# Kernel optimization log

Measured on AMD Instinct MI355X. Metric: run time of the kernel, lower is better.

## Reference

```python
import jax, jax.numpy as jnp
import numpy as np

EMB, HID, SEQ = 768, 512, 2048
BATCH = 2
EPS = 1e-6
LN_EPS = 1e-5
ROPE_BASE = 10000.0
NEG_BIG = -1e9  # stands in for -inf diagonal mask (identical entmax output, NaN-safe)


def rotate_half(x):
    d = x.shape[-1] // 2
    return jnp.concatenate([-x[..., d:], x[..., :d]], axis=-1)


def rope_tables(L, D, dtype=jnp.float32):
    inv_freq = 1.0 / (ROPE_BASE ** (jnp.arange(0, D, 2, dtype=jnp.float32) / D))
    t = jnp.arange(L, dtype=jnp.float32)
    freqs = jnp.outer(t, inv_freq)            # [L, D/2]
    emb = jnp.concatenate([freqs, freqs], -1)  # [L, D]
    return jnp.cos(emb).astype(dtype), jnp.sin(emb).astype(dtype)


def layernorm(x, gamma, beta):
    mu = jnp.mean(x, axis=-1, keepdims=True)
    var = jnp.mean(jnp.square(x - mu), axis=-1, keepdims=True)
    return (x - mu) * jax.lax.rsqrt(var + LN_EPS) * gamma + beta


def entmax15(z):
    """Exact 1.5-entmax along last axis (Peters & Martins sort algorithm)."""
    z = z / 2.0
    z = z - jnp.max(z, axis=-1, keepdims=True)
    zs = -jnp.sort(-z, axis=-1)                      # descending
    L = z.shape[-1]
    k = jnp.arange(1, L + 1, dtype=z.dtype)
    cum = jnp.cumsum(zs, axis=-1)
    cum2 = jnp.cumsum(zs * zs, axis=-1)
    mean = cum / k
    ss = cum2 - cum * mean                           # k*(E[x^2]-E[x]^2)
    delta = (1.0 - ss) / k
    tau = mean - jnp.sqrt(jnp.maximum(delta, 0.0))
    support = jnp.sum((tau <= zs).astype(jnp.int32), axis=-1)
    tau_star = jnp.take_along_axis(tau, (support - 1)[..., None], axis=-1)
    return jnp.square(jnp.maximum(z - tau_star, 0.0))


def setup_inputs() -> dict:
    key = jax.random.key(0)
    ks = jax.random.split(key, 3)
    x = jax.random.normal(ks[0], (BATCH, SEQ, EMB), dtype=jnp.float32)
    Wq = jax.random.normal(ks[1], (HID, EMB), dtype=jnp.float32) / np.sqrt(EMB)
    Wk = jax.random.normal(ks[2], (HID, EMB), dtype=jnp.float32) / np.sqrt(EMB)
    return {
        "x": x, "Wq": Wq, "Wk": Wk,
        "q_gamma": jnp.ones((HID,), jnp.float32), "q_beta": jnp.zeros((HID,), jnp.float32),
        "k_gamma": jnp.ones((HID,), jnp.float32), "k_beta": jnp.zeros((HID,), jnp.float32),
        "C_weight": jnp.ones((1,), jnp.float32),
        "F_weight": jnp.ones((1,), jnp.float32),
        "S_weight": jnp.ones((1,), jnp.float32),
    }


def reference(x, Wq, Wk, q_gamma, q_beta, k_gamma, k_beta, C_weight, F_weight, S_weight):
    B, L, _ = x.shape
    q = layernorm(x @ Wq.T, q_gamma, q_beta)   # [B,L,D]
    k = layernorm(x @ Wk.T, k_gamma, k_beta)
    cos, sin = rope_tables(L, q.shape[-1], q.dtype)
    q = q * cos + rotate_half(q) * sin
    k = k * cos + rotate_half(k) * sin

    wC = 2.0 * jax.nn.sigmoid(C_weight)
    wF = 2.0 * jax.nn.sigmoid(F_weight)
    wS = 2.0 * jax.nn.sigmoid(S_weight)

    Gkk = jnp.einsum('bld,ble->bde', k, k)     # [B,D,D]
    Gkq = jnp.einsum('bld,ble->bde', k, q)
    Gqq = jnp.einsum('bld,ble->bde', q, q)

    C_raw = jnp.einsum('bid,bde,bje->bij', q, Gkk, q)  # [B,L,L]
    F_raw = jnp.einsum('bid,bde,bje->bij', q, Gkq, k)
    S_raw = jnp.einsum('bid,bde,bje->bij', k, Gqq, k)

    C = C_raw - jnp.mean(C_raw, axis=-1, keepdims=True)
    Fm = F_raw - jnp.mean(F_raw, axis=-1, keepdims=True)
    S = S_raw - jnp.mean(S_raw, axis=-1, keepdims=True)

    pC = jnp.clip(entmax15(wC * C), 0.0, 1.0 - EPS)
    pF = jnp.clip(entmax15(wF * Fm), 0.0, 1.0 - EPS)
    pS = jnp.clip(entmax15(wS * S), 0.0, 1.0 - EPS)

    pC = pC * jax.lax.rsqrt(jnp.sum(pC, axis=-2, keepdims=True) + EPS)
    pS = pS * jax.lax.rsqrt(jnp.sum(pS, axis=-2, keepdims=True) + EPS)

    pC = jnp.maximum((1.0 - 2.0 * EPS) * pC + EPS, EPS)
    pF = jnp.maximum((1.0 - 2.0 * EPS) * pF + EPS, EPS)
    pS = jnp.maximum((1.0 - 2.0 * EPS) * pS + EPS, EPS)

    H = (jnp.log(pC) + jnp.log(pF) + jnp.log(pS)) / 3.0
    diag = jnp.eye(L, dtype=bool)[None]
    H = jnp.where(diag, NEG_BIG, H)
    H = entmax15(H)
    return H, pC, pF, pS
```

## Files before the change

kernel.cpp:

```cpp
#include <hip/hip_runtime.h>
#include <cstddef>
#include <math.h>

#define B_   2
#define L_   2048
#define D_   512
#define E_   768
static const size_t LL   = (size_t)L_ * L_;
static const size_t SLOT = (size_t)B_ * LL;

#define QK_N  ((size_t)B_ * L_ * D_)
#define G1_N  ((size_t)512 * 512)
#define G_N   ((size_t)6 * G1_N)
#define U_N   ((size_t)6 * L_ * D_)
#define X_N   ((size_t)4096 * 768)
#define W_N   ((size_t)512 * 768)

typedef unsigned short u16;
typedef __attribute__((ext_vector_type(8))) _Float16 half8;
typedef __attribute__((ext_vector_type(4))) float f32x4;

__device__ __forceinline__ void split2(float f, u16& h0, u16& h1) {
    _Float16 a = (_Float16)f;
    _Float16 b = (_Float16)((f - (float)a) * 4096.0f);
    h0 = __builtin_bit_cast(u16, a);
    h1 = __builtin_bit_cast(u16, b);
}

typedef const __attribute__((address_space(1))) void gas_void;
typedef __attribute__((address_space(3))) void las_void;

__device__ __forceinline__ void gload16(const u16* g, u16* l) {
    __builtin_amdgcn_global_load_lds((gas_void*)g, (las_void*)l, 16, 0, 0);
}

__device__ __forceinline__ void gemm12864p(const u16* __restrict__ Ap, size_t Aps, int lda,
                                           const u16* __restrict__ Bp, size_t Bps, int ldb,
                                           int K, int m0, int n0, int tid,
                                           double outv[4][2][4]) {
    __shared__ u16 SA[2][128][32], SB[2][64][32];
    f32x4 accH[4][2], accM[4][2];
#pragma unroll
    for (int i = 0; i < 4; ++i)
#pragma unroll
        for (int j = 0; j < 2; ++j) {
            accH[i][j] = (f32x4){0.f, 0.f, 0.f, 0.f};
            accM[i][j] = (f32x4){0.f, 0.f, 0.f, 0.f};
        }
    double accD[4][2][4] = {};
    int lane = tid & 63, w = tid >> 6;
    int wm = (w & 1) << 6, wn = (w >> 1) << 5;
    int fr = lane & 15, ko8 = lane >> 4;

    int rbA0 = (w << 5), rbA1 = (w << 5) + 16;
    int rowA0 = rbA0 + (lane >> 2), rowA1 = rbA1 + (lane >> 2);
    int chA0 = (lane & 3) ^ ((rowA0 >> 1) & 3);
    int chA1 = (lane & 3) ^ ((rowA1 >> 1) & 3);
    int rbB = (w << 4);
    int rowB = rbB + (lane >> 2);
    int chB = (lane & 3) ^ ((rowB >> 1) & 3);

    int nstep = K >> 5;
    for (int s = 0; s < nstep; ++s) {
        int k0 = s << 5;
#pragma unroll
        for (int sp = 0; sp < 2; ++sp) {
            gload16(Ap + (size_t)sp * Aps + (size_t)(m0 + rowA0) * lda + k0 + (chA0 << 3),
                    &SA[sp][rbA0][0]);
            gload16(Ap + (size_t)sp * Aps + (size_t)(m0 + rowA1) * lda + k0 + (chA1 << 3),
                    &SA[sp][rbA1][0]);
            gload16(Bp + (size_t)sp * Bps + (size_t)(n0 + rowB) * ldb + k0 + (chB << 3),
                    &SB[sp][rbB][0]);
        }
        __syncthreads();
        half8 a[4][2], b[2][2];
#pragma unroll
        for (int f = 0; f < 4; ++f) {
            int ra = wm + (f << 4) + fr;
            int ca = (ko8 ^ ((ra >> 1) & 3)) << 3;
#pragma unroll
            for (int sp = 0; sp < 2; ++sp)
                a[f][sp] = *reinterpret_cast<const half8*>(&SA[sp][ra][ca]);
        }
#pragma unroll
        for (int f = 0; f < 2; ++f) {
            int rbn = wn + (f << 4) + fr;
            int cb = (ko8 ^ ((rbn >> 1) & 3)) << 3;
#pragma unroll
            for (int sp = 0; sp < 2; ++sp)
                b[f][sp] = *reinterpret_cast<const half8*>(&SB[sp][rbn][cb]);
        }
#pragma unroll
        for (int fi = 0; fi < 4; ++fi)
#pragma unroll
            for (int fj = 0; fj < 2; ++fj) {
                accH[fi][fj] = __builtin_amdgcn_mfma_f32_16x16x32_f16(a[fi][0], b[fj][0], accH[fi][fj], 0, 0, 0);
                accM[fi][fj] = __builtin_amdgcn_mfma_f32_16x16x32_f16(a[fi][0], b[fj][1], accM[fi][fj], 0, 0, 0);
                accM[fi][fj] = __builtin_amdgcn_mfma_f32_16x16x32_f16(a[fi][1], b[fj][0], accM[fi][fj], 0, 0, 0);
            }
        __syncthreads();
#pragma unroll
        for (int fi = 0; fi < 4; ++fi)
#pragma unroll
            for (int fj = 0; fj < 2; ++fj) {
#pragma unroll
                for (int r = 0; r < 4; ++r) accD[fi][fj][r] += (double)accH[fi][fj][r];
                accH[fi][fj] = (f32x4){0.f, 0.f, 0.f, 0.f};
            }
    }
    const double S1 = 1.0 / 4096.0;
#pragma unroll
    for (int fi = 0; fi < 4; ++fi)
#pragma unroll
        for (int fj = 0; fj < 2; ++fj)
#pragma unroll
            for (int r = 0; r < 4; ++r)
                outv[fi][fj][r] = accD[fi][fj][r] + (double)accM[fi][fj][r] * S1;
}

__device__ __forceinline__ void gstage128(const u16* __restrict__ P, size_t pstride, int ld,
                                          int r0, int k0, int lane, int w,
                                          u16 S[2][128][32]) {
#pragma unroll
    for (int sp = 0; sp < 2; ++sp)
#pragma unroll
        for (int t = 0; t < 2; ++t) {
            int rb = (w << 5) + (t << 4);
            int row = rb + (lane >> 2);
            int chunk = (lane & 3) ^ ((row >> 1) & 3);
            const u16* src = P + (size_t)sp * pstride + (size_t)(r0 + row) * ld
                             + (k0 + (chunk << 3));
            gload16(src, &S[sp][rb][0]);
        }
}

__device__ __forceinline__ void gemm128(const u16* __restrict__ Ap, size_t Aps, int lda,
                                        const u16* __restrict__ Bp, size_t Bps, int ldb,
                                        int K, int m0, int n0, int tid,
                                        float* __restrict__ out, int ldo) {
    __shared__ u16 SA[2][128][32], SB[2][128][32];
    f32x4 accH[4][4], accM[4][4];
#pragma unroll
    for (int i = 0; i < 4; ++i)
#pragma unroll
        for (int j = 0; j < 4; ++j) {
            accH[i][j] = (f32x4){0.f, 0.f, 0.f, 0.f};
            accM[i][j] = (f32x4){0.f, 0.f, 0.f, 0.f};
        }
    int lane = tid & 63, w = tid >> 6;
    int wm = (w & 1) << 6, wn = (w >> 1) << 6;
    int fr = lane & 15, ko8 = lane >> 4;

    int nstep = K >> 5;
    for (int s = 0; s < nstep; ++s) {
        int k0 = s << 5;
        gstage128(Ap, Aps, lda, m0, k0, lane, w, SA);
        gstage128(Bp, Bps, ldb, n0, k0, lane, w, SB);
        __syncthreads();
        half8 a[4][2], b[4][2];
#pragma unroll
        for (int f = 0; f < 4; ++f) {
            int ra = wm + (f << 4) + fr;
            int rbn = wn + (f << 4) + fr;
            int ca = (ko8 ^ ((ra >> 1) & 3)) << 3;
            int cb = (ko8 ^ ((rbn >> 1) & 3)) << 3;
#pragma unroll
            for (int sp = 0; sp < 2; ++sp) {
                a[f][sp] = *reinterpret_cast<const half8*>(&SA[sp][ra][ca]);
                b[f][sp] = *reinterpret_cast<const half8*>(&SB[sp][rbn][cb]);
            }
        }
#pragma unroll
        for (int fi = 0; fi < 4; ++fi)
#pragma unroll
            for (int fj = 0; fj < 4; ++fj) {
                accH[fi][fj] = __builtin_amdgcn_mfma_f32_16x16x32_f16(a[fi][0], b[fj][0], accH[fi][fj], 0, 0, 0);
                accM[fi][fj] = __builtin_amdgcn_mfma_f32_16x16x32_f16(a[fi][0], b[fj][1], accM[fi][fj], 0, 0, 0);
                accM[fi][fj] = __builtin_amdgcn_mfma_f32_16x16x32_f16(a[fi][1], b[fj][0], accM[fi][fj], 0, 0, 0);
            }
        __syncthreads();
    }
    const double S1 = 1.0 / 4096.0;
    int col = lane & 15, rbase = (lane >> 4) << 2;
#pragma unroll
    for (int fi = 0; fi < 4; ++fi)
#pragma unroll
        for (int fj = 0; fj < 4; ++fj)
#pragma unroll
            for (int r = 0; r < 4; ++r) {
                int mm = m0 + wm + (fi << 4) + rbase + r;
                int nn = n0 + wn + (fj << 4) + col;
                out[(size_t)mm * ldo + nn] =
                    (float)((double)accH[fi][fj][r] + (double)accM[fi][fj][r] * S1);
            }
}

__global__ __launch_bounds__(256) void k_prep(const float* __restrict__ x,
                                              const float* __restrict__ Wq,
                                              const float* __restrict__ Wk,
                                              u16* __restrict__ xP,
                                              u16* __restrict__ WP,
                                              double* __restrict__ tg) {
    int bx = blockIdx.x;
    if (bx < L_) {
        int l = bx, j = threadIdx.x;
        double e = (double)j * (1.0 / 256.0);
        double inv = pow(10000.0, -e);
        double ang = (double)l * inv;
        tg[(size_t)l * 512 + j] = cos(ang);
        tg[(size_t)l * 512 + 256 + j] = sin(ang);
        return;
    }
    size_t gid = (size_t)(bx - L_) * 256 + threadIdx.x;
    const size_t XH = X_N / 2, WH = W_N / 2;
    const float* src; u16* dst; size_t pn, off;
    if (gid < XH)            { src = x  + 2 * gid;              dst = xP;            pn = X_N; off = 2 * gid; }
    else if (gid < XH + WH)  { size_t g = gid - XH;      src = Wq + 2 * g; dst = WP;            pn = W_N; off = 2 * g; }
    else                     { size_t g = gid - XH - WH; src = Wk + 2 * g; dst = WP + 2 * W_N;  pn = W_N; off = 2 * g; }
    float2 v = *reinterpret_cast<const float2*>(src);
    u16 a0, a1, b0, b1;
    split2(v.x, a0, a1);
    split2(v.y, b0, b1);
    *reinterpret_cast<unsigned*>(dst + off)      = (unsigned)a0 | ((unsigned)b0 << 16);
    *reinterpret_cast<unsigned*>(dst + pn + off) = (unsigned)a1 | ((unsigned)b1 << 16);
}

__global__ __launch_bounds__(256, 2) void k_proj(const u16* __restrict__ xP,
                                                 const u16* __restrict__ WP,
                                                 float* __restrict__ qraw,
                                                 float* __restrict__ kraw) {
    int z = blockIdx.z;
    float* out = z ? kraw : qraw;
    const u16* Bp = WP + (size_t)z * 2 * W_N;
    gemm128(xP, X_N, E_, Bp, W_N, E_, E_,
            blockIdx.y * 128, blockIdx.x * 128, threadIdx.x, out, D_);
}

__global__ __launch_bounds__(256) void k_lnrope(const float* __restrict__ qraw,
                                                const float* __restrict__ kraw,
                                                const double* __restrict__ tg,
                                                const float* __restrict__ qg, const float* __restrict__ qb,
                                                const float* __restrict__ kg, const float* __restrict__ kb,
                                                u16* __restrict__ qP, u16* __restrict__ kP) {
    int row = blockIdx.x;
    int l = row & (L_ - 1);
    int tid = threadIdx.x;
    int half = tid >> 7, t = tid & 127;
    __shared__ double nrow[2][D_];
    __shared__ double red[8];
    __shared__ double cs_[256], sn_[256];
    {
        int j = tid & 255;
        if (tid < 256) { cs_[j] = tg[(size_t)l * 512 + j]; sn_[j] = tg[(size_t)l * 512 + 256 + j]; }
    }
    const float* rp = (half ? kraw : qraw) + (size_t)row * D_;
    const float* g  = half ? kg : qg;
    const float* bt = half ? kb : qb;
    u16* P = half ? kP : qP;
    float4 v = reinterpret_cast<const float4*>(rp)[t];
    double vv[4] = {(double)v.x, (double)v.y, (double)v.z, (double)v.w};
    double s = vv[0] + vv[1] + vv[2] + vv[3];
    double s2 = vv[0]*vv[0] + vv[1]*vv[1] + vv[2]*vv[2] + vv[3]*vv[3];
    for (int off = 32; off; off >>= 1) { s += __shfl_xor(s, off); s2 += __shfl_xor(s2, off); }
    int wv = tid >> 6;
    if ((tid & 63) == 0) { red[wv * 2] = s; red[wv * 2 + 1] = s2; }
    __syncthreads();
    double mu  = (red[half * 4 + 0] + red[half * 4 + 2]) * (1.0 / D_);
    double var = (red[half * 4 + 1] + red[half * 4 + 3]) * (1.0 / D_) - mu * mu;
    double rs = rsqrt(var + 1e-5);
    int d0 = t * 4;
    double o[4];
#pragma unroll
    for (int c = 0; c < 4; ++c) {
        int d = d0 + c;
        o[c] = (vv[c] - mu) * rs * (double)g[d] + (double)bt[d];
    }
#pragma unroll
    for (int c = 0; c < 4; ++c) nrow[half][d0 + c] = o[c];
    __syncthreads();
    u16 h[2][4];
#pragma unroll
    for (int c = 0; c < 4; ++c) {
        int d = d0 + c;
        double rot = (d < 256) ? -nrow[half][d + 256] : nrow[half][d - 256];
        float ov = (float)(nrow[half][d] * cs_[d & 255] + rot * sn_[d & 255]);
        split2(ov, h[0][c], h[1][c]);
    }
    size_t off = (size_t)row * D_ + d0;
#pragma unroll
    for (int sp = 0; sp < 2; ++sp)
        *reinterpret_cast<ushort4*>(P + sp * QK_N + off) = make_ushort4(h[sp][0], h[sp][1], h[sp][2], h[sp][3]);
}

__global__ __launch_bounds__(256) void k_qkT(const u16* __restrict__ qP,
                                             const u16* __restrict__ kP,
                                             u16* __restrict__ qPT,
                                             u16* __restrict__ kPT) {
    __shared__ u16 T[64][72];
    int z = blockIdx.z;
    int b = z & 1, sp = (z >> 1) & 1, tn = z >> 2;
    const u16* src = (tn ? kP : qP) + (size_t)sp * QK_N + (size_t)b * L_ * D_;
    u16* dst       = (tn ? kPT : qPT) + (size_t)sp * QK_N + (size_t)b * D_ * L_;
    int l0 = blockIdx.x * 64, d0 = blockIdx.y * 64;
    int tid = threadIdx.x;
#pragma unroll
    for (int i = 0; i < 2; ++i) {
        int idx = tid + i * 256;
        int lr = idx >> 3, dc8 = (idx & 7) << 3;
        *reinterpret_cast<uint4*>(&T[lr][dc8]) =
            *reinterpret_cast<const uint4*>(&src[(size_t)(l0 + lr) * D_ + d0 + dc8]);
    }
    __syncthreads();
#pragma unroll
    for (int i = 0; i < 2; ++i) {
        int idx = tid + i * 256;
        int dr = idx >> 3, lc8 = (idx & 7) << 3;
        u16 tmp[8];
#pragma unroll
        for (int c = 0; c < 8; ++c) tmp[c] = T[lc8 + c][dr];
        *reinterpret_cast<uint4*>(&dst[(size_t)(d0 + dr) * L_ + l0 + lc8]) =
            *reinterpret_cast<const uint4*>(tmp);
    }
}

__global__ __launch_bounds__(256, 2) void k_gram(const u16* __restrict__ qPT,
                                                 const u16* __restrict__ kPT,
                                                 float* __restrict__ Gpart) {
    int zz = blockIdx.z, half = zz & 1, z = zz >> 1;
    int b = z / 3, m = z % 3;
    const u16* A  = ((m == 2) ? qPT : kPT) + (size_t)b * D_ * L_ + (size_t)half * (L_ / 2);
    const u16* Bp = ((m == 0) ? kPT : qPT) + (size_t)b * D_ * L_ + (size_t)half * (L_ / 2);
    int m0 = blockIdx.y * 128, n0 = blockIdx.x * 64;
    double ov[4][2][4];
    gemm12864p(A, QK_N, L_, Bp, QK_N, L_, L_ / 2, m0, n0, threadIdx.x, ov);
    float* Gg = Gpart + (size_t)half * G_N + (size_t)z * G1_N;
    int lane = threadIdx.x & 63, w = threadIdx.x >> 6;
    int wm = (w & 1) << 6, wn = (w >> 1) << 5;
    int col = lane & 15, rbase = (lane >> 4) << 2;
#pragma unroll
    for (int fi = 0; fi < 4; ++fi)
#pragma unroll
        for (int fj = 0; fj < 2; ++fj)
#pragma unroll
            for (int r = 0; r < 4; ++r) {
                int mm = m0 + wm + fi * 16 + rbase + r;
                int nn = n0 + wn + fj * 16 + col;
                Gg[(size_t)mm * 512 + nn] = (float)ov[fi][fj][r];
            }
}

__global__ __launch_bounds__(256) void k_gsplitT(const float* __restrict__ Gpart,
                                                 u16* __restrict__ GPT) {
    __shared__ float T[64][65];
    int z = blockIdx.z, d0 = blockIdx.y * 64, e0 = blockIdx.x * 64;
    const float* Ga = Gpart + (size_t)z * G1_N;
    const float* Gb = Ga + G_N;
    int tid = threadIdx.x;
#pragma unroll
    for (int i = 0; i < 16; ++i) {
        int idx = tid + i * 256;
        int r = idx >> 6, c = idx & 63;
        size_t o = (size_t)(d0 + r) * 512 + e0 + c;
        T[r][c] = Ga[o] + Gb[o];
    }
    __syncthreads();
    u16* Gz = GPT + (size_t)z * G1_N;
#pragma unroll
    for (int i = 0; i < 16; ++i) {
        int idx = tid + i * 256;
        int er = idx >> 6, dc = idx & 63;
        u16 h0, h1; split2(T[dc][er], h0, h1);
        size_t o = (size_t)(e0 + er) * 512 + d0 + dc;
        Gz[o] = h0; Gz[G_N + o] = h1;
    }
}

__global__ __launch_bounds__(256, 2) void k_u(const u16* __restrict__ qP,
                                              const u16* __restrict__ kP,
                                              const u16* __restrict__ GPT,
                                              u16* __restrict__ UP) {
    int z = blockIdx.z, b = z / 3, m = z % 3;
    const u16* A  = ((m == 2) ? kP : qP) + (size_t)b * L_ * D_;
    const u16* Bp = GPT + (size_t)z * G1_N;
    int m0 = blockIdx.y * 128, n0 = blockIdx.x * 64;
    double ov[4][2][4];
    gemm12864p(A, QK_N, D_, Bp, G_N, 512, D_, m0, n0, threadIdx.x, ov);
    int lane = threadIdx.x & 63, w = threadIdx.x >> 6;
    int wm = (w & 1) << 6, wn = (w >> 1) << 5;
    int col = lane & 15, rbase = (lane >> 4) << 2;
#pragma unroll
    for (int fi = 0; fi < 4; ++fi)
#pragma unroll
        for (int fj = 0; fj < 2; ++fj)
#pragma unroll
            for (int r = 0; r < 4; ++r) {
                float uf = (float)ov[fi][fj][r];
                int mm = m0 + wm + fi * 16 + rbase + r;
                int nn = n0 + wn + fj * 16 + col;
                size_t off = (size_t)z * ((size_t)L_ * D_) + (size_t)mm * D_ + nn;
                u16 h0, h1; split2(uf, h0, h1);
                UP[off] = h0; UP[U_N + off] = h1;
            }
}

__global__ __launch_bounds__(256, 2) void k_scores(const u16* __restrict__ qP,
                                                   const u16* __restrict__ kP,
                                                   const u16* __restrict__ UP,
                                                   float* __restrict__ out) {
    int bid = blockIdx.x;
    int swz = (bid & 7) * 192 + (bid >> 3);
    int z = swz >> 8, rem = swz & 255;
    int by = rem >> 4, bx = rem & 15;
    int b = z / 3, m = z % 3;
    const u16* A  = UP + (size_t)z * ((size_t)L_ * D_);
    const u16* Bp = ((m == 0) ? qP : kP) + (size_t)b * L_ * D_;
    float* Co = out + (size_t)(1 + m) * SLOT + (size_t)b * LL;
    gemm128(A, U_N, D_, Bp, QK_N, D_, D_,
            by * 128, bx * 128, threadIdx.x, Co, L_);
}

__global__ __launch_bounds__(256) void k_entmax(float* __restrict__ base, int nrows,
                                                const float* __restrict__ wC,
                                                const float* __restrict__ wF,
                                                const float* __restrict__ wS) {
    int tid = threadIdx.x;
    int lane = tid & 63;
    int r = blockIdx.x * 4 + (tid >> 6);
    if (r >= nrows) return;
    int m = r >> 12;
    const float* wp = (m == 0) ? wC : (m == 1) ? wF : wS;
    float hw = (float)(1.0 / (1.0 + exp(-(double)wp[0])));
    float* row = base + (size_t)r * L_;
    float v[32];
    float mx = -3.4e38f;
#pragma unroll
    for (int j = 0; j < 32; ++j) {
        v[j] = row[lane + (j << 6)];
        mx = fmaxf(mx, v[j]);
    }
    for (int off = 32; off; off >>= 1) mx = fmaxf(mx, __shfl_xor(mx, off));
    float z[32];
#pragma unroll
    for (int j = 0; j < 32; ++j) z[j] = hw * (v[j] - mx);
    float lo = -1.0f, hi = 0.0f;
    for (int it = 0; it < 9; ++it) {
        float tau = 0.5f * (lo + hi);
        float ssum = 0.0f;
#pragma unroll
        for (int j = 0; j < 32; ++j) {
            float t = fmaxf(z[j] - tau, 0.0f);
            ssum = fmaf(t, t, ssum);
        }
        for (int off = 32; off; off >>= 1) ssum += __shfl_xor(ssum, off);
        if (ssum >= 1.0f) lo = tau; else hi = tau;
    }
    float tau = lo;
    for (int it = 0; it < 3; ++it) {
        float s1 = 0.0f, s2 = 0.0f;
#pragma unroll
        for (int j = 0; j < 32; ++j) {
            float t = fmaxf(z[j] - tau, 0.0f);
            s1 += t;
            s2 = fmaf(t, t, s2);
        }
        for (int off = 32; off; off >>= 1) { s1 += __shfl_xor(s1, off); s2 += __shfl_xor(s2, off); }
        float denom = 2.0f * s1;
        if (denom > 1e-30f) tau += fmaxf((s2 - 1.0f) / denom, 0.0f);
    }
#pragma unroll
    for (int j = 0; j < 32; ++j) {
        float t = fmaxf(z[j] - tau, 0.0f);
        row[lane + (j << 6)] = fminf(t * t, 1.0f - 1e-6f);
    }
}

__global__ __launch_bounds__(256) void k_colsum(const float* __restrict__ out,
                                                double* __restrict__ part) {
    int bz = blockIdx.z, which = bz >> 1, b = bz & 1;
    const float* mat = out + (size_t)(which ? 3 : 1) * SLOT + (size_t)b * LL;
    int j = blockIdx.x * 256 + threadIdx.x;
    int r0 = blockIdx.y * 128;
    double s = 0.0;
#pragma unroll 8
    for (int r = 0; r < 128; ++r) s += (double)mat[(size_t)(r0 + r) * L_ + j];
    part[((size_t)bz * 16 + blockIdx.y) * L_ + j] = s;
}

__global__ __launch_bounds__(256) void k_colred(const double* __restrict__ part,
                                                double* __restrict__ csC,
                                                double* __restrict__ csS) {
    int g = blockIdx.x * 256 + threadIdx.x;
    int bz = g >> 11, j = g & (L_ - 1);
    int which = bz >> 1, b = bz & 1;
    double s = 0.0;
#pragma unroll
    for (int c = 0; c < 16; ++c) s += part[((size_t)bz * 16 + c) * L_ + j];
    (which ? csS : csC)[b * L_ + j] = s;
}

__global__ __launch_bounds__(256) void k_fin2(float* __restrict__ out,
                                              const double* __restrict__ csC,
                                              const double* __restrict__ csS) {
    int row = blockIdx.x;
    int i = row & (L_ - 1), b = row >> 11;
    size_t ro = (size_t)row * L_;
    float* H  = out + ro;
    float* pC = out + SLOT + ro;
    float* pF = out + 2 * SLOT + ro;
    float* pS = out + 3 * SLOT + ro;
    const double* cc = csC + b * L_;
    const double* cs = csS + b * L_;
    int tid = threadIdx.x, lane = tid & 63, wv = tid >> 6;
    __shared__ float red[4], red2[4];
    const double A1 = 1.0 - 2e-6;
    float h[8];
    float mx = -3.4e38f;
#pragma unroll
    for (int c = 0; c < 8; ++c) {
        int j = (c << 8) + tid;
        double cv = (double)pC[j] * rsqrt(cc[j] + 1e-6);
        double fv = (double)pF[j];
        double sv = (double)pS[j] * rsqrt(cs[j] + 1e-6);
        cv = fmax(A1 * cv + 1e-6, 1e-6);
        fv = fmax(A1 * fv + 1e-6, 1e-6);
        sv = fmax(A1 * sv + 1e-6, 1e-6);
        pC[j] = (float)cv; pF[j] = (float)fv; pS[j] = (float)sv;
        h[c] = (j == i) ? -1e9f : logf((float)(cv * fv * sv)) * (1.0f / 3.0f);
        mx = fmaxf(mx, h[c]);
    }
    for (int off = 32; off; off >>= 1) mx = fmaxf(mx, __shfl_xor(mx, off));
    if (lane == 0) red[wv] = mx;
    __syncthreads();
    mx = fmaxf(fmaxf(red[0], red[1]), fmaxf(red[2], red[3]));
    __syncthreads();
    float z[8];
#pragma unroll
    for (int c = 0; c < 8; ++c) z[c] = 0.5f * (h[c] - mx);
    float lo = -1.0f, hi = 0.0f;
    for (int it = 0; it < 9; ++it) {
        float tau = 0.5f * (lo + hi);
        float ssum = 0.0f;
#pragma unroll
        for (int c = 0; c < 8; ++c) {
            float t = fmaxf(z[c] - tau, 0.0f);
            ssum = fmaf(t, t, ssum);
        }
        for (int off = 32; off; off >>= 1) ssum += __shfl_xor(ssum, off);
        if (lane == 0) red[wv] = ssum;
        __syncthreads();
        ssum = red[0] + red[1] + red[2] + red[3];
        __syncthreads();
        if (ssum >= 1.0f) lo = tau; else hi = tau;
    }
    float tau = lo;
    for (int it = 0; it < 3; ++it) {
        float s1 = 0.0f, s2 = 0.0f;
#pragma unroll
        for (int c = 0; c < 8; ++c) {
            float t = fmaxf(z[c] - tau, 0.0f);
            s1 += t;
            s2 = fmaf(t, t, s2);
        }
        for (int off = 32; off; off >>= 1) { s1 += __shfl_xor(s1, off); s2 += __shfl_xor(s2, off); }
        if (lane == 0) { red[wv] = s1; red2[wv] = s2; }
        __syncthreads();
        s1 = red[0] + red[1] + red[2] + red[3];
        s2 = red2[0] + red2[1] + red2[2] + red2[3];
        __syncthreads();
        float denom = 2.0f * s1;
        if (denom > 1e-30f) tau += fmaxf((s2 - 1.0f) / denom, 0.0f);
    }
#pragma unroll
    for (int c = 0; c < 8; ++c) {
        float t = fmaxf(z[c] - tau, 0.0f);
        H[(c << 8) + tid] = t * t;
    }
}

extern "C" void kernel_launch(void* const* d_in, const int* in_sizes, int n_in,
                              void* d_out, int out_size, void* d_ws, size_t ws_size,
                              hipStream_t stream) {
    const float* x  = (const float*)d_in[0];
    const float* Wq = (const float*)d_in[1];
    const float* Wk = (const float*)d_in[2];
    const float* qg = (const float*)d_in[3];
    const float* qb = (const float*)d_in[4];
    const float* kg = (const float*)d_in[5];
    const float* kb = (const float*)d_in[6];
    const float* wC = (const float*)d_in[7];
    const float* wF = (const float*)d_in[8];
    const float* wS = (const float*)d_in[9];
    float* out = (float*)d_out;

    char* wsb = (char*)d_ws;
    u16*    UP   = (u16*)wsb;
    float*  qraw = (float*)wsb;
    float*  kraw = qraw + QK_N;
    u16*    qPT  = (u16*)wsb;
    u16*    kPT  = qPT + 2 * QK_N;
    float*  Gpart = (float*)(wsb + 2 * QK_N * sizeof(float));
    wsb += 3 * U_N * sizeof(u16);
    u16*    qP    = (u16*)wsb;
    u16*    xP    = (u16*)wsb;   wsb += 3 * QK_N * sizeof(u16);
    u16*    kP    = (u16*)wsb;   wsb += 3 * QK_N * sizeof(u16);
    u16*    GPT   = (u16*)wsb;
    u16*    WP    = (u16*)wsb;   wsb += 3 * G_N * sizeof(u16);
    double* tg    = (double*)wsb;
    double* part  = tg;
    double* csC   = tg + (size_t)4 * 16 * L_;
    double* csS   = csC + (size_t)B_ * L_;

    k_prep    <<<dim3(L_ + 7680), 256, 0, stream>>>(x, Wq, Wk, xP, WP, tg);
    k_proj    <<<dim3(4, 32, 2),  256, 0, stream>>>(xP, WP, qraw, kraw);
    k_lnrope  <<<dim3(B_ * L_),   256, 0, stream>>>(qraw, kraw, tg, qg, qb, kg, kb, qP, kP);
    k_qkT     <<<dim3(32, 8, 8),  256, 0, stream>>>(qP, kP, qPT, kPT);
    k_gram    <<<dim3(8, 4, 12),  256, 0, stream>>>(qPT, kPT, Gpart);
    k_gsplitT <<<dim3(8, 8, 6),   256, 0, stream>>>(Gpart, GPT);
    k_u       <<<dim3(8, 16, 6),  256, 0, stream>>>(qP, kP, GPT, UP);
    k_scores  <<<dim3(1536),      256, 0, stream>>>(qP, kP, UP, out);
    k_entmax  <<<dim3(3072),      256, 0, stream>>>(out + SLOT, 3 * B_ * L_, wC, wF, wS);
    k_colsum  <<<dim3(8, 16, 4),  256, 0, stream>>>(out, part);
    k_colred  <<<dim3(32),        256, 0, stream>>>(part, csC, csS);
    k_fin2    <<<dim3(B_ * L_),   256, 0, stream>>>(out, csC, csS);
}
```

Baseline: 455.7 us.

## Double-buffer GEMM LDS tiles with 512-thread blocks and BK=64 prefetch

Replaces the single-buffered 128x128 split-fp16 GEMM with a double-buffered variant. It uses 512 threads per block (8 waves, each computing 64x32), a K-step of 64, and issues global-to-LDS loads for the next tile while MFMAs run on the current one. The aim is to hide global load latency and halve the number of barriers, at the cost of 64KB of LDS and one block per CU. The block-id swizzle for L2 locality in the scores kernel is dropped in favour of a plain 3D grid.

New measurement: 463.9 us. About the same (+1.8%).

```diff
diff --git a/kernel.cpp b/kernel.cpp
--- a/kernel.cpp
+++ b/kernel.cpp
@@ -118,66 +118,94 @@
                 outv[fi][fj][r] = accD[fi][fj][r] + (double)accM[fi][fj][r] * S1;
 }
 
-__device__ __forceinline__ void gstage128(const u16* __restrict__ P, size_t pstride, int ld,
-                                          int r0, int k0, int lane, int w,
-                                          u16 S[2][128][32]) {
-#pragma unroll
-    for (int sp = 0; sp < 2; ++sp)
-#pragma unroll
-        for (int t = 0; t < 2; ++t) {
-            int rb = (w << 5) + (t << 4);
-            int row = rb + (lane >> 2);
-            int chunk = (lane & 3) ^ ((row >> 1) & 3);
-            const u16* src = P + (size_t)sp * pstride + (size_t)(r0 + row) * ld
-                             + (k0 + (chunk << 3));
-            gload16(src, &S[sp][rb][0]);
-        }
-}
-
-__device__ __forceinline__ void gemm128(const u16* __restrict__ Ap, size_t Aps, int lda,
-                                        const u16* __restrict__ Bp, size_t Bps, int ldb,
-                                        int K, int m0, int n0, int tid,
-                                        float* __restrict__ out, int ldo) {
-    __shared__ u16 SA[2][128][32], SB[2][128][32];
-    f32x4 accH[4][4], accM[4][4];
+__device__ __forceinline__ void stage_round(const u16* __restrict__ Ap, size_t Aps, int lda, int m0,
+                                            const u16* __restrict__ Bp, size_t Bps, int ldb, int n0,
+                                            int k0, int q, int tid,
+                                            u16* SAb, u16* SBb) {
+    int idx = (q << 9) + tid;
+    int op = idx >> 11;
+    int r  = idx & 2047;
+    int pl = r >> 10, ks = (r >> 9) & 1, row = (r >> 2) & 127, ch = r & 3;
+    int csrc = ch ^ ((row >> 1) & 3);
+    const u16* src = (op ? Bp + (size_t)pl * Bps + (size_t)(n0 + row) * ldb
+                         : Ap + (size_t)pl * Aps + (size_t)(m0 + row) * lda)
+                     + k0 + (ks << 5) + (csrc << 3);
+    int rw = (idx & ~63) - (op << 11);
+    u16* base = (op ? SBb : SAb) + ((size_t)rw << 3);
+    gload16(src, base);
+}
+
+__device__ __forceinline__ void gemm128p2(const u16* __restrict__ Ap, size_t Aps, int lda,
+                                          const u16* __restrict__ Bp, size_t Bps, int ldb,
+                                          int K, int m0, int n0, int tid,
+                                          float* __restrict__ out, int ldo) {
+    __shared__ u16 SA[2][2][2][128][32];
+    __shared__ u16 SB[2][2][2][128][32];
+    f32x4 accH[4][2], accM[4][2];
 #pragma unroll
     for (int i = 0; i < 4; ++i)
 #pragma unroll
-        for (int j = 0; j < 4; ++j) {
+        for (int j = 0; j < 2; ++j) {
             accH[i][j] = (f32x4){0.f, 0.f, 0.f, 0.f};
             accM[i][j] = (f32x4){0.f, 0.f, 0.f, 0.f};
         }
     int lane = tid & 63, w = tid >> 6;
-    int wm = (w & 1) << 6, wn = (w >> 1) << 6;
+    int wm = (w & 1) << 6, wn = (w >> 1) << 5;
     int fr = lane & 15, ko8 = lane >> 4;
 
-    int nstep = K >> 5;
-    for (int s = 0; s < nstep; ++s) {
-        int k0 = s << 5;
-        gstage128(Ap, Aps, lda, m0, k0, lane, w, SA);
-        gstage128(Bp, Bps, ldb, n0, k0, lane, w, SB);
-        __syncthreads();
-        half8 a[4][2], b[4][2];
-#pragma unroll
-        for (int f = 0; f < 4; ++f) {
-            int ra = wm + (f << 4) + fr;
-            int rbn = wn + (f << 4) + fr;
-            int ca = (ko8 ^ ((ra >> 1) & 3)) << 3;
-            int cb = (ko8 ^ ((rbn >> 1) & 3)) << 3;
-#pragma unroll
-            for (int sp = 0; sp < 2; ++sp) {
-                a[f][sp] = *reinterpret_cast<const half8*>(&SA[sp][ra][ca]);
-                b[f][sp] = *reinterpret_cast<const half8*>(&SB[sp][rbn][cb]);
+#pragma unroll
+    for (int q = 0; q < 8; ++q)
+        stage_round(Ap, Aps, lda, m0, Bp, Bps, ldb, n0, 0, q, tid,
+                    &SA[0][0][0][0][0], &SB[0][0][0][0][0]);
+    asm volatile("s_waitcnt vmcnt(0)" ::: "memory");
+    __syncthreads();
+
+    int ntile = K >> 6;
+    for (int t = 0; t < ntile; ++t) {
+        int cur = t & 1, nxt = cur ^ 1;
+        int k1 = (t + 1) << 6;
+        bool more = (t + 1) < ntile;
+        u16* SAn = &SA[nxt][0][0][0][0];
+        u16* SBn = &SB[nxt][0][0][0][0];
+#pragma unroll
+        for (int ks = 0; ks < 2; ++ks) {
+            half8 bb[2][2];
+#pragma unroll
+            for (int nf = 0; nf < 2; ++nf) {
+                int rbn = wn + (nf << 4) + fr;
+                int cb = (ko8 ^ ((rbn >> 1) & 3)) << 3;
+                bb[nf][0] = *reinterpret_cast<const half8*>(&SB[cur][0][ks][rbn][cb]);
+                bb[nf][1] = *reinterpret_cast<const half8*>(&SB[cur][1][ks][rbn][cb]);
             }
-        }
-#pragma unroll
-        for (int fi = 0; fi < 4; ++fi)
-#pragma unroll
-            for (int fj = 0; fj < 4; ++fj) {
-                accH[fi][fj] = __builtin_amdgcn_mfma_f32_16x16x32_f16(a[fi][0], b[fj][0], accH[fi][fj], 0, 0, 0);
-                accM[fi][fj] = __builtin_amdgcn_mfma_f32_16x16x32_f16(a[fi][0], b[fj][1], accM[fi][fj], 0, 0, 0);
-                accM[fi][fj] = __builtin_amdgcn_mfma_f32_16x16x32_f16(a[fi][1], b[fj][0], accM[fi][fj], 0, 0, 0);
+#pragma unroll
+            for (int mh = 0; mh < 2; ++mh) {
+                int q = (ks << 1) + mh;
+                if (more) {
+                    stage_round(Ap, Aps, lda, m0, Bp, Bps, ldb, n0, k1, 2 * q,     tid, SAn, SBn);
+                    stage_round(Ap, Aps, lda, m0, Bp, Bps, ldb, n0, k1, 2 * q + 1, tid, SAn, SBn);
+                }
+                half8 aa[2][2];
+#pragma unroll
+                for (int mf = 0; mf < 2; ++mf) {
+                    int fi = (mh << 1) + mf;
+                    int ra = wm + (fi << 4) + fr;
+                    int ca = (ko8 ^ ((ra >> 1) & 3)) << 3;
+                    aa[mf][0] = *reinterpret_cast<const half8*>(&SA[cur][0][ks][ra][ca]);
+                    aa[mf][1] = *reinterpret_cast<const half8*>(&SA[cur][1][ks][ra][ca]);
+                }
+#pragma unroll
+                for (int mf = 0; mf < 2; ++mf) {
+                    int fi = (mh << 1) + mf;
+#pragma unroll
+                    for (int nf = 0; nf < 2; ++nf) {
+                        accH[fi][nf] = __builtin_amdgcn_mfma_f32_16x16x32_f16(aa[mf][0], bb[nf][0], accH[fi][nf], 0, 0, 0);
+                        accM[fi][nf] = __builtin_amdgcn_mfma_f32_16x16x32_f16(aa[mf][0], bb[nf][1], accM[fi][nf], 0, 0, 0);
+                        accM[fi][nf] = __builtin_amdgcn_mfma_f32_16x16x32_f16(aa[mf][1], bb[nf][0], accM[fi][nf], 0, 0, 0);
+                    }
+                }
             }
+        }
+        asm volatile("s_waitcnt vmcnt(0)" ::: "memory");
         __syncthreads();
     }
     const double S1 = 1.0 / 4096.0;
@@ -185,7 +213,7 @@
 #pragma unroll
     for (int fi = 0; fi < 4; ++fi)
 #pragma unroll
-        for (int fj = 0; fj < 4; ++fj)
+        for (int fj = 0; fj < 2; ++fj)
 #pragma unroll
             for (int r = 0; r < 4; ++r) {
                 int mm = m0 + wm + (fi << 4) + rbase + r;
@@ -225,15 +253,15 @@
     *reinterpret_cast<unsigned*>(dst + pn + off) = (unsigned)a1 | ((unsigned)b1 << 16);
 }
 
-__global__ __launch_bounds__(256, 2) void k_proj(const u16* __restrict__ xP,
+__global__ __launch_bounds__(512, 1) void k_proj(const u16* __restrict__ xP,
                                                  const u16* __restrict__ WP,
                                                  float* __restrict__ qraw,
                                                  float* __restrict__ kraw) {
     int z = blockIdx.z;
     float* out = z ? kraw : qraw;
     const u16* Bp = WP + (size_t)z * 2 * W_N;
-    gemm128(xP, X_N, E_, Bp, W_N, E_, E_,
-            blockIdx.y * 128, blockIdx.x * 128, threadIdx.x, out, D_);
+    gemm128p2(xP, X_N, E_, Bp, W_N, E_, E_,
+              blockIdx.y * 128, blockIdx.x * 128, threadIdx.x, out, D_);
 }
 
 __global__ __launch_bounds__(256) void k_lnrope(const float* __restrict__ qraw,
@@ -403,20 +431,16 @@
             }
 }
 
-__global__ __launch_bounds__(256, 2) void k_scores(const u16* __restrict__ qP,
+__global__ __launch_bounds__(512, 1) void k_scores(const u16* __restrict__ qP,
                                                    const u16* __restrict__ kP,
                                                    const u16* __restrict__ UP,
                                                    float* __restrict__ out) {
-    int bid = blockIdx.x;
-    int swz = (bid & 7) * 192 + (bid >> 3);
-    int z = swz >> 8, rem = swz & 255;
-    int by = rem >> 4, bx = rem & 15;
-    int b = z / 3, m = z % 3;
+    int z = blockIdx.z, b = z / 3, m = z % 3;
     const u16* A  = UP + (size_t)z * ((size_t)L_ * D_);
     const u16* Bp = ((m == 0) ? qP : kP) + (size_t)b * L_ * D_;
     float* Co = out + (size_t)(1 + m) * SLOT + (size_t)b * LL;
-    gemm128(A, U_N, D_, Bp, QK_N, D_, D_,
-            by * 128, bx * 128, threadIdx.x, Co, L_);
+    gemm128p2(A, U_N, D_, Bp, QK_N, D_, D_,
+              blockIdx.y * 128, blockIdx.x * 128, threadIdx.x, Co, L_);
 }
 
 __global__ __launch_bounds__(256) void k_entmax(float* __restrict__ base, int nrows,
@@ -611,13 +635,13 @@
     double* csS   = csC + (size_t)B_ * L_;
 
     k_prep    <<<dim3(L_ + 7680), 256, 0, stream>>>(x, Wq, Wk, xP, WP, tg);
-    k_proj    <<<dim3(4, 32, 2),  256, 0, stream>>>(xP, WP, qraw, kraw);
+    k_proj    <<<dim3(4, 32, 2),  512, 0, stream>>>(xP, WP, qraw, kraw);
     k_lnrope  <<<dim3(B_ * L_),   256, 0, stream>>>(qraw, kraw, tg, qg, qb, kg, kb, qP, kP);
     k_qkT     <<<dim3(32, 8, 8),  256, 0, stream>>>(qP, kP, qPT, kPT);
     k_gram    <<<dim3(8, 4, 12),  256, 0, stream>>>(qPT, kPT, Gpart);
     k_gsplitT <<<dim3(8, 8, 6),   256, 0, stream>>>(Gpart, GPT);
     k_u       <<<dim3(8, 16, 6),  256, 0, stream>>>(qP, kP, GPT, UP);
-    k_scores  <<<dim3(1536),      256, 0, stream>>>(qP, kP, UP, out);
+    k_scores  <<<dim3(16, 16, 6), 512, 0, stream>>>(qP, kP, UP, out);
     k_entmax  <<<dim3(3072),      256, 0, stream>>>(out + SLOT, 3 * B_ * L_, wC, wF, wS);
     k_colsum  <<<dim3(8, 16, 4),  256, 0, stream>>>(out, part);
     k_colred  <<<dim3(32),        256, 0, stream>>>(part, csC, csS);
```
